# Performance work log

Measured on AMD Instinct MI355X. Metric: run time of the kernel, lower is better.

Reference implementation:

```python
import jax, jax.numpy as jnp
import numpy as np

IN_F = 4096
OUT_F = 11008
RANK = 16
LORA_SCALE = 2.0
VALS_PER_WORD = 16


def pack_int2(T):
    """Pack ternary T in {-1,0,+1} [out, in] into int32 [out, in//16] (code = T+1)."""
    out_f, in_f = T.shape
    codes = (T + 1).astype(jnp.int32).reshape(out_f, in_f // VALS_PER_WORD, VALS_PER_WORD)
    shifts = (jnp.arange(VALS_PER_WORD, dtype=jnp.int32) * 2)
    # disjoint bit fields -> sum == bitwise OR
    return jnp.sum(codes << shifts, axis=-1).astype(jnp.int32)


def unpack_int2(packed, in_features, dtype):
    """Unpack int32 [out, nblk] -> ternary [out, in_features] in given dtype."""
    shifts = (jnp.arange(VALS_PER_WORD, dtype=jnp.int32) * 2)
    codes = (packed[:, :, None] >> shifts) & 3  # [out, nblk, 16]
    T = codes.reshape(packed.shape[0], -1)[:, :in_features]
    return T.astype(dtype) - jnp.asarray(1, dtype)


def setup_inputs() -> dict:
    key = jax.random.key(0)
    k_x, k_t, k_a, k_m, k_b, k_la, k_lb = jax.random.split(key, 7)
    x = jax.random.normal(k_x, (256, IN_F), dtype=jnp.float32)
    # random ternary weights, packed faithfully (code = T + 1)
    T = jax.random.randint(k_t, (OUT_F, IN_F), -1, 2, dtype=jnp.int32)
    int2_packed = pack_int2(T)
    alpha = jax.random.uniform(k_a, (OUT_F,), dtype=jnp.float32, minval=0.01, maxval=0.05)
    mu = jax.random.normal(k_m, (OUT_F,), dtype=jnp.float32) * 0.001
    bias = jax.random.normal(k_b, (OUT_F,), dtype=jnp.float32) * 0.02
    lora_A = jax.random.normal(k_la, (RANK, IN_F), dtype=jnp.float32) * (1.0 / np.sqrt(IN_F))
    lora_B = jax.random.normal(k_lb, (OUT_F, RANK), dtype=jnp.float32) * 0.01
    return {"x": x, "int2_packed": int2_packed, "alpha": alpha, "mu": mu,
            "bias": bias, "lora_A": lora_A, "lora_B": lora_B}


def reference(x, int2_packed, alpha, mu, bias, lora_A, lora_B):
    # unpack INT2 -> ternary weight matrix in activation dtype
    T = unpack_int2(int2_packed, IN_F, x.dtype)          # [out, in]
    ternary_out = jnp.einsum('mi,oi->mo', x, T)          # F.linear(x, T)
    ternary_out = ternary_out * alpha                    # per-row scale
    # asymmetric shift: mu_o * sum_i x_i
    ternary_out = ternary_out + mu * jnp.sum(x, axis=-1, keepdims=True)
    # LoRA correction: scale * (x A^T) B^T
    lora_out = jnp.einsum('mr,or->mo', jnp.einsum('mi,ri->mr', x, lora_A), lora_B)
    ternary_out = ternary_out + LORA_SCALE * lora_out
    return ternary_out + bias
```

## Files before the change

### kernel.cpp

```cpp
#include <hip/hip_runtime.h>
#include <stdint.h>

#define IN_F 4096
#define OUT_F 11008
#define M_ROWS 256
#define RANK 16
#define NWORDS 256

#define BM 128
#define BN 64
#define BK 64
#define KSPLIT 2
#define K_PER 2048
#define NIT 32

typedef unsigned short u16;
typedef __attribute__((ext_vector_type(8))) short short8;
typedef __attribute__((ext_vector_type(4))) float floatx4;

__device__ __forceinline__ u16 f32_to_bf16_rne(float f) {
    uint32_t u = __builtin_bit_cast(uint32_t, f);
    uint32_t r = (u + 0x7FFFu + ((u >> 16) & 1u)) >> 16;
    return (u16)r;
}

__global__ __launch_bounds__(256) void prep_kernel(
    const float* __restrict__ x, const float* __restrict__ lora_A,
    u16* __restrict__ xb, float* __restrict__ srow, float* __restrict__ lxa)
{
    const int m = blockIdx.x;
    const int tid = threadIdx.x;
    const float4* xrow4 = (const float4*)(x + (size_t)m * IN_F);
    const float4* la4 = (const float4*)lora_A;
    float ssum = 0.f;
    float acc[RANK];
#pragma unroll
    for (int r = 0; r < RANK; ++r) acc[r] = 0.f;
#pragma unroll
    for (int t = 0; t < IN_F / (256 * 4); ++t) {
        int i4 = t * 256 + tid;
        float4 v = xrow4[i4];
        ssum += v.x + v.y + v.z + v.w;
        union { u16 h[4]; uint2 u2; } pk;
        pk.h[0] = f32_to_bf16_rne(v.x);
        pk.h[1] = f32_to_bf16_rne(v.y);
        pk.h[2] = f32_to_bf16_rne(v.z);
        pk.h[3] = f32_to_bf16_rne(v.w);
        *(uint2*)&xb[(size_t)m * IN_F + i4 * 4] = pk.u2;
#pragma unroll
        for (int r = 0; r < RANK; ++r) {
            float4 a = la4[r * (IN_F / 4) + i4];
            acc[r] = fmaf(v.x, a.x, fmaf(v.y, a.y, fmaf(v.z, a.z, fmaf(v.w, a.w, acc[r]))));
        }
    }
#pragma unroll
    for (int off = 32; off > 0; off >>= 1) {
        ssum += __shfl_down(ssum, off, 64);
#pragma unroll
        for (int r = 0; r < RANK; ++r) acc[r] += __shfl_down(acc[r], off, 64);
    }
    __shared__ float red[4][RANK + 1];
    int wv = tid >> 6, ln = tid & 63;
    if (ln == 0) {
        red[wv][0] = ssum;
#pragma unroll
        for (int r = 0; r < RANK; ++r) red[wv][1 + r] = acc[r];
    }
    __syncthreads();
    if (tid == 0) srow[m] = red[0][0] + red[1][0] + red[2][0] + red[3][0];
    if (tid < RANK)
        lxa[m * RANK + tid] = red[0][1 + tid] + red[1][1 + tid] + red[2][1 + tid] + red[3][1 + tid];
}

__global__ __launch_bounds__(256) void init_kernel(
    const float* __restrict__ mu,
    const float* __restrict__ bias, const float* __restrict__ lora_B,
    const float* __restrict__ srow, const float* __restrict__ lxa,
    float* __restrict__ out)
{
    const int tid = threadIdx.x;
    const int o = blockIdx.x * 256 + tid;
    const int m0 = blockIdx.y * 32;
    float bi = bias[o];
    float muv = mu[o];
    float Br[RANK];
    const float4* b4 = (const float4*)(lora_B + (size_t)o * RANK);
#pragma unroll
    for (int r4 = 0; r4 < RANK / 4; ++r4) {
        float4 v = b4[r4];
        Br[r4 * 4 + 0] = v.x; Br[r4 * 4 + 1] = v.y;
        Br[r4 * 4 + 2] = v.z; Br[r4 * 4 + 3] = v.w;
    }
    __shared__ float ss[32];
    __shared__ float slx[32][RANK];
    if (tid < 32) ss[tid] = srow[m0 + tid];
    for (int t = tid; t < 32 * RANK; t += 256)
        slx[t >> 4][t & 15] = lxa[(m0 + (t >> 4)) * RANK + (t & 15)];
    __syncthreads();
#pragma unroll 4
    for (int mm = 0; mm < 32; ++mm) {
        float dot = 0.f;
#pragma unroll
        for (int r = 0; r < RANK; ++r) dot = fmaf(slx[mm][r], Br[r], dot);
        out[(size_t)(m0 + mm) * OUT_F + o] = bi + muv * ss[mm] + 2.0f * dot;
    }
}

__device__ __forceinline__ short8 decode8(uint32_t h)
{
    uint32_t selA = (h & 0xFu) | ((h & 0xF0u) << 12);
    selA = (selA | (selA << 6)) & 0x03030303u;
    uint32_t h2 = h >> 8;
    uint32_t selB = (h2 & 0xFu) | ((h2 & 0xF0u) << 12);
    selB = (selB | (selB << 6)) & 0x03030303u;
    uint32_t hiA = __builtin_amdgcn_perm(0u, 0x003F00BFu, selA);
    uint32_t loA = __builtin_amdgcn_perm(0u, 0x00800080u, selA);
    uint32_t hiB = __builtin_amdgcn_perm(0u, 0x003F00BFu, selB);
    uint32_t loB = __builtin_amdgcn_perm(0u, 0x00800080u, selB);
    union { uint32_t u[4]; short8 s; } cvt;
    cvt.u[0] = __builtin_amdgcn_perm(hiA, loA, 0x05010400u);
    cvt.u[1] = __builtin_amdgcn_perm(hiA, loA, 0x07030602u);
    cvt.u[2] = __builtin_amdgcn_perm(hiB, loB, 0x05010400u);
    cvt.u[3] = __builtin_amdgcn_perm(hiB, loB, 0x07030602u);
    return cvt.s;
}

#define WAITV5 asm volatile("s_waitcnt vmcnt(5)" ::: "memory")
#define WAITV0 asm volatile("s_waitcnt vmcnt(0)" ::: "memory")
#define BAR    __builtin_amdgcn_s_barrier()
#define SCHED0 __builtin_amdgcn_sched_barrier(0)

struct Frags {
    short8 af[4][2];
    uint32_t bwd[2][2];
};

__global__ __launch_bounds__(256, 3) void gemm_kernel(
    const u16* __restrict__ xb, const uint32_t* __restrict__ Tp,
    const float* __restrict__ alpha, float* __restrict__ out)
{
    __shared__ __align__(16) u16 ldsA[3][BM * BK];
    __shared__ __align__(16) uint32_t ldsB[3][BN * 4];

    const int tid = threadIdx.x;
    const int lane = tid & 63;
    const int wave = tid >> 6;
    const int wm = wave >> 1, wn = wave & 1;
    const int mb = blockIdx.y * BM;
    const int nb = blockIdx.x * BN;
    const int z = blockIdx.z;

    const int bshift = ((lane >> 4) & 1) * 16;

    const u16* asrc[4];
    int adst[4];
#pragma unroll
    for (int i = 0; i < 4; ++i) {
        int q = i * 256 + tid;
        int row = q >> 3;
        int scc = (q & 7) ^ (row & 7);
        asrc[i] = xb + (size_t)(mb + row) * IN_F + z * K_PER + scc * 8;
        adst[i] = q * 8;
    }
    const uint32_t* bsrc = Tp + (size_t)(nb + lane) * NWORDS + z * (K_PER / 16);
    const int bdst = lane * 4;

    int aoff[4][2], boff[2][2];
#pragma unroll
    for (int mt = 0; mt < 4; ++mt)
#pragma unroll
        for (int kk = 0; kk < 2; ++kk) {
            int r = wm * 64 + mt * 16 + (lane & 15);
            int sc = kk * 4 + (lane >> 4);
            aoff[mt][kk] = (r * 8 + (sc ^ (r & 7))) * 8;
        }
#pragma unroll
    for (int nt = 0; nt < 2; ++nt)
#pragma unroll
        for (int kk = 0; kk < 2; ++kk) {
            int row = wn * 32 + nt * 16 + (lane & 15);
            boff[nt][kk] = row * 4 + kk * 2 + (lane >> 5);
        }

    floatx4 acc[4][2] = {};

    auto stage = [&](int buf, int jt) {
#pragma unroll
        for (int i = 0; i < 4; ++i) {
            __builtin_amdgcn_global_load_lds(
                (const __attribute__((address_space(1))) void*)(asrc[i] + jt * BK),
                (__attribute__((address_space(3))) void*)(&ldsA[buf][adst[i]]),
                16, 0, 0);
        }
        __builtin_amdgcn_global_load_lds(
            (const __attribute__((address_space(1))) void*)(bsrc + jt * 4),
            (__attribute__((address_space(3))) void*)(&ldsB[buf][bdst]),
            16, 0, 0);
    };

    auto rdfrags = [&](int buf, Frags& F) {
#pragma unroll
        for (int mt = 0; mt < 4; ++mt)
#pragma unroll
            for (int kk = 0; kk < 2; ++kk)
                F.af[mt][kk] = *(const short8*)&ldsA[buf][aoff[mt][kk]];
#pragma unroll
        for (int nt = 0; nt < 2; ++nt)
#pragma unroll
            for (int kk = 0; kk < 2; ++kk)
                F.bwd[nt][kk] = ldsB[buf][boff[nt][kk]];
    };

    auto compute = [&](Frags& F) {
        __builtin_amdgcn_s_setprio(1);
#pragma unroll
        for (int kk = 0; kk < 2; ++kk) {
#pragma unroll
            for (int nt = 0; nt < 2; ++nt) {
                short8 bf = decode8((F.bwd[nt][kk] >> bshift) & 0xFFFFu);
#pragma unroll
                for (int mt = 0; mt < 4; ++mt)
                    acc[mt][nt] = __builtin_amdgcn_mfma_f32_16x16x32_bf16(
                        F.af[mt][kk], bf, acc[mt][nt], 0, 0, 0);
            }
        }
        __builtin_amdgcn_s_setprio(0);
    };

    Frags fA, fB;

    stage(0, 0);
    stage(1, 1);
    WAITV5; BAR;
    rdfrags(0, fA); SCHED0;

#pragma unroll 1
    for (int u = 0; u < 5; ++u) {
        const int j = u * 6;
        stage(2, j + 2); SCHED0; compute(fA); WAITV5; BAR; rdfrags(1, fB); SCHED0;
        stage(0, j + 3); SCHED0; compute(fB); WAITV5; BAR; rdfrags(2, fA); SCHED0;
        stage(1, j + 4); SCHED0; compute(fA); WAITV5; BAR; rdfrags(0, fB); SCHED0;
        stage(2, j + 5); SCHED0; compute(fB); WAITV5; BAR; rdfrags(1, fA); SCHED0;
        stage(0, j + 6); SCHED0; compute(fA); WAITV5; BAR; rdfrags(2, fB); SCHED0;
        stage(1, j + 7); SCHED0; compute(fB); WAITV5; BAR; rdfrags(0, fA); SCHED0;
    }
    WAITV0; compute(fA); BAR; rdfrags(1, fB); SCHED0;
    compute(fB);

    const int o0 = nb + wn * 32 + (lane & 15);
    const int m0 = mb + wm * 64 + ((lane >> 4) * 4);
    float al[2] = { alpha[o0], alpha[o0 + 16] };
#pragma unroll
    for (int mt = 0; mt < 4; ++mt) {
#pragma unroll
        for (int rg = 0; rg < 4; ++rg) {
            int m = m0 + mt * 16 + rg;
#pragma unroll
            for (int nt = 0; nt < 2; ++nt)
                atomicAdd(&out[(size_t)m * OUT_F + o0 + nt * 16],
                          al[nt] * acc[mt][nt][rg]);
        }
    }
}

extern "C" void kernel_launch(void* const* d_in, const int* in_sizes, int n_in,
                              void* d_out, int out_size, void* d_ws, size_t ws_size,
                              hipStream_t stream)
{
    const float* x = (const float*)d_in[0];
    const uint32_t* Tp = (const uint32_t*)d_in[1];
    const float* alpha = (const float*)d_in[2];
    const float* mu = (const float*)d_in[3];
    const float* bias = (const float*)d_in[4];
    const float* lora_A = (const float*)d_in[5];
    const float* lora_B = (const float*)d_in[6];
    float* out = (float*)d_out;

    u16* xb = (u16*)d_ws;
    float* srow = (float*)((char*)d_ws + (size_t)M_ROWS * IN_F * 2);
    float* lxa = (float*)((char*)d_ws + (size_t)M_ROWS * IN_F * 2 + 4096);

    prep_kernel<<<dim3(M_ROWS), dim3(256), 0, stream>>>(x, lora_A, xb, srow, lxa);
    init_kernel<<<dim3(OUT_F / 256, M_ROWS / 32), dim3(256), 0, stream>>>(
        mu, bias, lora_B, srow, lxa, out);
    gemm_kernel<<<dim3(OUT_F / BN, M_ROWS / BM, KSPLIT), dim3(256), 0, stream>>>(
        xb, Tp, alpha, out);
}
```

Baseline: 66.04 us.

## Transpose packed weights into coalesced layout, load B to registers, fuse epilogue

A new pack kernel runs on every call and re-lays the packed ternary weights so that consecutive output columns are contiguous per k-word pair. The GEMM can then read B fragments straight from global memory into registers instead of staging them through LDS. The separate init kernel is replaced by a memset plus a fused epilogue in the z==0 split, which adds mu*rowsum, the LoRA term and the bias before its atomic add. This drops the full-output init write pass and the LDS traffic for B, but adds a transpose kernel and a memset each call and lengthens the epilogue of half the blocks.

```diff
diff --git a/kernel.cpp b/kernel.cpp
--- a/kernel.cpp
+++ b/kernel.cpp
@@ -72,37 +72,27 @@
         lxa[m * RANK + tid] = red[0][1 + tid] + red[1][1 + tid] + red[2][1 + tid] + red[3][1 + tid];
 }
 
-__global__ __launch_bounds__(256) void init_kernel(
-    const float* __restrict__ mu,
-    const float* __restrict__ bias, const float* __restrict__ lora_B,
-    const float* __restrict__ srow, const float* __restrict__ lxa,
-    float* __restrict__ out)
-{
+__global__ __launch_bounds__(256) void pack_kernel(
+    const uint32_t* __restrict__ Tp, uint2* __restrict__ Tw2)
+{
+    __shared__ uint32_t s[64][NWORDS + 1];
     const int tid = threadIdx.x;
-    const int o = blockIdx.x * 256 + tid;
-    const int m0 = blockIdx.y * 32;
-    float bi = bias[o];
-    float muv = mu[o];
-    float Br[RANK];
-    const float4* b4 = (const float4*)(lora_B + (size_t)o * RANK);
-#pragma unroll
-    for (int r4 = 0; r4 < RANK / 4; ++r4) {
-        float4 v = b4[r4];
-        Br[r4 * 4 + 0] = v.x; Br[r4 * 4 + 1] = v.y;
-        Br[r4 * 4 + 2] = v.z; Br[r4 * 4 + 3] = v.w;
-    }
-    __shared__ float ss[32];
-    __shared__ float slx[32][RANK];
-    if (tid < 32) ss[tid] = srow[m0 + tid];
-    for (int t = tid; t < 32 * RANK; t += 256)
-        slx[t >> 4][t & 15] = lxa[(m0 + (t >> 4)) * RANK + (t & 15)];
+    const int col0 = blockIdx.x * 64;
+#pragma unroll 8
+    for (int i = 0; i < 64; ++i) {
+        int idx = i * 256 + tid;
+        s[idx >> 8][idx & 255] = Tp[(size_t)(col0 + (idx >> 8)) * NWORDS + (idx & 255)];
+    }
     __syncthreads();
-#pragma unroll 4
-    for (int mm = 0; mm < 32; ++mm) {
-        float dot = 0.f;
-#pragma unroll
-        for (int r = 0; r < RANK; ++r) dot = fmaf(slx[mm][r], Br[r], dot);
-        out[(size_t)(m0 + mm) * OUT_F + o] = bi + muv * ss[mm] + 2.0f * dot;
+    const int c = tid & 63;
+#pragma unroll 8
+    for (int q = 0; q < 32; ++q) {
+        int wq = q * 4 + (tid >> 6);
+        int t = wq >> 1, p = wq & 1;
+        uint2 v;
+        v.x = s[c][4 * t + p];
+        v.y = s[c][4 * t + 2 + p];
+        Tw2[(size_t)wq * OUT_F + col0 + c] = v;
     }
 }
 
@@ -125,22 +115,22 @@
     return cvt.s;
 }
 
-#define WAITV5 asm volatile("s_waitcnt vmcnt(5)" ::: "memory")
+#define WAITV6 asm volatile("s_waitcnt vmcnt(6)" ::: "memory")
 #define WAITV0 asm volatile("s_waitcnt vmcnt(0)" ::: "memory")
 #define BAR    __builtin_amdgcn_s_barrier()
 #define SCHED0 __builtin_amdgcn_sched_barrier(0)
 
-struct Frags {
-    short8 af[4][2];
-    uint32_t bwd[2][2];
-};
+struct Frags { short8 af[4][2]; };
+struct BW    { uint2 w[2]; };
 
 __global__ __launch_bounds__(256, 3) void gemm_kernel(
-    const u16* __restrict__ xb, const uint32_t* __restrict__ Tp,
-    const float* __restrict__ alpha, float* __restrict__ out)
+    const u16* __restrict__ xb, const uint2* __restrict__ Tw2,
+    const float* __restrict__ alpha, const float* __restrict__ mu,
+    const float* __restrict__ bias, const float* __restrict__ lora_B,
+    const float* __restrict__ srow, const float* __restrict__ lxa,
+    float* __restrict__ out)
 {
     __shared__ __align__(16) u16 ldsA[3][BM * BK];
-    __shared__ __align__(16) uint32_t ldsB[3][BN * 4];
 
     const int tid = threadIdx.x;
     const int lane = tid & 63;
@@ -162,10 +152,13 @@
         asrc[i] = xb + (size_t)(mb + row) * IN_F + z * K_PER + scc * 8;
         adst[i] = q * 8;
     }
-    const uint32_t* bsrc = Tp + (size_t)(nb + lane) * NWORDS + z * (K_PER / 16);
-    const int bdst = lane * 4;
-
-    int aoff[4][2], boff[2][2];
+    const uint2* bptr[2];
+#pragma unroll
+    for (int nt = 0; nt < 2; ++nt)
+        bptr[nt] = Tw2 + (size_t)(z * 64 + (lane >> 5)) * OUT_F
+                       + nb + wn * 32 + nt * 16 + (lane & 15);
+
+    int aoff[4][2];
 #pragma unroll
     for (int mt = 0; mt < 4; ++mt)
 #pragma unroll
@@ -173,13 +166,6 @@
             int r = wm * 64 + mt * 16 + (lane & 15);
             int sc = kk * 4 + (lane >> 4);
             aoff[mt][kk] = (r * 8 + (sc ^ (r & 7))) * 8;
-        }
-#pragma unroll
-    for (int nt = 0; nt < 2; ++nt)
-#pragma unroll
-        for (int kk = 0; kk < 2; ++kk) {
-            int row = wn * 32 + nt * 16 + (lane & 15);
-            boff[nt][kk] = row * 4 + kk * 2 + (lane >> 5);
         }
 
     floatx4 acc[4][2] = {};
@@ -192,32 +178,27 @@
                 (__attribute__((address_space(3))) void*)(&ldsA[buf][adst[i]]),
                 16, 0, 0);
         }
-        __builtin_amdgcn_global_load_lds(
-            (const __attribute__((address_space(1))) void*)(bsrc + jt * 4),
-            (__attribute__((address_space(3))) void*)(&ldsB[buf][bdst]),
-            16, 0, 0);
     };
-
+    auto loadB = [&](BW& b, int jt) {
+#pragma unroll
+        for (int nt = 0; nt < 2; ++nt)
+            b.w[nt] = bptr[nt][(size_t)(2 * jt) * OUT_F];
+    };
     auto rdfrags = [&](int buf, Frags& F) {
 #pragma unroll
         for (int mt = 0; mt < 4; ++mt)
 #pragma unroll
             for (int kk = 0; kk < 2; ++kk)
                 F.af[mt][kk] = *(const short8*)&ldsA[buf][aoff[mt][kk]];
-#pragma unroll
-        for (int nt = 0; nt < 2; ++nt)
-#pragma unroll
-            for (int kk = 0; kk < 2; ++kk)
-                F.bwd[nt][kk] = ldsB[buf][boff[nt][kk]];
     };
-
-    auto compute = [&](Frags& F) {
+    auto compute = [&](Frags& F, BW& b) {
         __builtin_amdgcn_s_setprio(1);
 #pragma unroll
         for (int kk = 0; kk < 2; ++kk) {
 #pragma unroll
             for (int nt = 0; nt < 2; ++nt) {
-                short8 bf = decode8((F.bwd[nt][kk] >> bshift) & 0xFFFFu);
+                uint32_t w = kk ? b.w[nt].y : b.w[nt].x;
+                short8 bf = decode8((w >> bshift) & 0xFFFFu);
 #pragma unroll
                 for (int mt = 0; mt < 4; ++mt)
                     acc[mt][nt] = __builtin_amdgcn_mfma_f32_16x16x32_bf16(
@@ -228,37 +209,79 @@
     };
 
     Frags fA, fB;
-
-    stage(0, 0);
-    stage(1, 1);
-    WAITV5; BAR;
+    BW bw0, bw1, bw2;
+
+    stage(0, 0); loadB(bw0, 0);
+    WAITV0; BAR;
     rdfrags(0, fA); SCHED0;
+    loadB(bw1, 1); stage(1, 1);
 
 #pragma unroll 1
     for (int u = 0; u < 5; ++u) {
         const int j = u * 6;
-        stage(2, j + 2); SCHED0; compute(fA); WAITV5; BAR; rdfrags(1, fB); SCHED0;
-        stage(0, j + 3); SCHED0; compute(fB); WAITV5; BAR; rdfrags(2, fA); SCHED0;
-        stage(1, j + 4); SCHED0; compute(fA); WAITV5; BAR; rdfrags(0, fB); SCHED0;
-        stage(2, j + 5); SCHED0; compute(fB); WAITV5; BAR; rdfrags(1, fA); SCHED0;
-        stage(0, j + 6); SCHED0; compute(fA); WAITV5; BAR; rdfrags(2, fB); SCHED0;
-        stage(1, j + 7); SCHED0; compute(fB); WAITV5; BAR; rdfrags(0, fA); SCHED0;
-    }
-    WAITV0; compute(fA); BAR; rdfrags(1, fB); SCHED0;
-    compute(fB);
+        loadB(bw2, j + 2); stage(2, j + 2); SCHED0; compute(fA, bw0); WAITV6; BAR; rdfrags(1, fB); SCHED0;
+        loadB(bw0, j + 3); stage(0, j + 3); SCHED0; compute(fB, bw1); WAITV6; BAR; rdfrags(2, fA); SCHED0;
+        loadB(bw1, j + 4); stage(1, j + 4); SCHED0; compute(fA, bw2); WAITV6; BAR; rdfrags(0, fB); SCHED0;
+        loadB(bw2, j + 5); stage(2, j + 5); SCHED0; compute(fB, bw0); WAITV6; BAR; rdfrags(1, fA); SCHED0;
+        loadB(bw0, j + 6); stage(0, j + 6); SCHED0; compute(fA, bw1); WAITV6; BAR; rdfrags(2, fB); SCHED0;
+        loadB(bw1, j + 7); stage(1, j + 7); SCHED0; compute(fB, bw2); WAITV6; BAR; rdfrags(0, fA); SCHED0;
+    }
+    compute(fA, bw0); WAITV0; BAR; rdfrags(1, fB); SCHED0;
+    compute(fB, bw1);
 
     const int o0 = nb + wn * 32 + (lane & 15);
     const int m0 = mb + wm * 64 + ((lane >> 4) * 4);
     float al[2] = { alpha[o0], alpha[o0 + 16] };
-#pragma unroll
-    for (int mt = 0; mt < 4; ++mt) {
-#pragma unroll
-        for (int rg = 0; rg < 4; ++rg) {
-            int m = m0 + mt * 16 + rg;
-#pragma unroll
-            for (int nt = 0; nt < 2; ++nt)
-                atomicAdd(&out[(size_t)m * OUT_F + o0 + nt * 16],
-                          al[nt] * acc[mt][nt][rg]);
+
+    if (z == 0) {
+        float muv[2] = { mu[o0], mu[o0 + 16] };
+        float bi[2]  = { bias[o0], bias[o0 + 16] };
+        float Brow[2][RANK];
+#pragma unroll
+        for (int nt = 0; nt < 2; ++nt) {
+            const float4* b4 = (const float4*)(lora_B + (size_t)(o0 + nt * 16) * RANK);
+#pragma unroll
+            for (int r4 = 0; r4 < RANK / 4; ++r4) {
+                float4 v = b4[r4];
+                Brow[nt][r4 * 4 + 0] = v.x; Brow[nt][r4 * 4 + 1] = v.y;
+                Brow[nt][r4 * 4 + 2] = v.z; Brow[nt][r4 * 4 + 3] = v.w;
+            }
+        }
+#pragma unroll
+        for (int mt = 0; mt < 4; ++mt) {
+#pragma unroll
+            for (int rg = 0; rg < 4; ++rg) {
+                int m = m0 + mt * 16 + rg;
+                float sm = srow[m];
+                float lx[RANK];
+                const float4* l4 = (const float4*)(lxa + (size_t)m * RANK);
+#pragma unroll
+                for (int r4 = 0; r4 < RANK / 4; ++r4) {
+                    float4 v = l4[r4];
+                    lx[r4 * 4 + 0] = v.x; lx[r4 * 4 + 1] = v.y;
+                    lx[r4 * 4 + 2] = v.z; lx[r4 * 4 + 3] = v.w;
+                }
+#pragma unroll
+                for (int nt = 0; nt < 2; ++nt) {
+                    float lora = 0.f;
+#pragma unroll
+                    for (int r = 0; r < RANK; ++r) lora = fmaf(lx[r], Brow[nt][r], lora);
+                    atomicAdd(&out[(size_t)m * OUT_F + o0 + nt * 16],
+                              al[nt] * acc[mt][nt][rg] + muv[nt] * sm + 2.0f * lora + bi[nt]);
+                }
+            }
+        }
+    } else {
+#pragma unroll
+        for (int mt = 0; mt < 4; ++mt) {
+#pragma unroll
+            for (int rg = 0; rg < 4; ++rg) {
+                int m = m0 + mt * 16 + rg;
+#pragma unroll
+                for (int nt = 0; nt < 2; ++nt)
+                    atomicAdd(&out[(size_t)m * OUT_F + o0 + nt * 16],
+                              al[nt] * acc[mt][nt][rg]);
+            }
         }
     }
 }
@@ -279,10 +302,11 @@
     u16* xb = (u16*)d_ws;
     float* srow = (float*)((char*)d_ws + (size_t)M_ROWS * IN_F * 2);
     float* lxa = (float*)((char*)d_ws + (size_t)M_ROWS * IN_F * 2 + 4096);
-
+    uint2* Tw2 = (uint2*)((char*)d_ws + (4u << 20));
+
+    hipMemsetAsync(out, 0, (size_t)out_size * sizeof(float), stream);
     prep_kernel<<<dim3(M_ROWS), dim3(256), 0, stream>>>(x, lora_A, xb, srow, lxa);
-    init_kernel<<<dim3(OUT_F / 256, M_ROWS / 32), dim3(256), 0, stream>>>(
-        mu, bias, lora_B, srow, lxa, out);
+    pack_kernel<<<dim3(OUT_F / 64), dim3(256), 0, stream>>>(Tp, Tw2);
     gemm_kernel<<<dim3(OUT_F / BN, M_ROWS / BM, KSPLIT), dim3(256), 0, stream>>>(
-        xb, Tp, alpha, out);
-}
+        xb, Tw2, alpha, mu, bias, lora_B, srow, lxa, out);
+}
```

After: 73.54 us. +11.4%, slower.

## Repack ternary weights for direct register loads and widen GEMM tiles

Applied to the files above, without the earlier changes.

Adds a pack kernel that transposes the packed INT2 weights into a column-interleaved uint2 layout, so GEMM waves can load B words straight from global into registers instead of staging them through LDS. The GEMM tile widens to BN=128, split-K rises to 4 with a 4-deep A ring buffer, and occupancy drops to 2 blocks per SM. The repack runs on every call, which adds a kernel launch and extra weight traffic, and split-K 4 doubles the atomic output traffic.

```diff
diff --git a/kernel.cpp b/kernel.cpp
--- a/kernel.cpp
+++ b/kernel.cpp
@@ -8,11 +8,11 @@
 #define NWORDS 256
 
 #define BM 128
-#define BN 64
+#define BN 128
 #define BK 64
-#define KSPLIT 2
-#define K_PER 2048
-#define NIT 32
+#define KSPLIT 4
+#define K_PER 1024
+#define NIT 16
 
 typedef unsigned short u16;
 typedef __attribute__((ext_vector_type(8))) short short8;
@@ -70,6 +70,30 @@
     if (tid == 0) srow[m] = red[0][0] + red[1][0] + red[2][0] + red[3][0];
     if (tid < RANK)
         lxa[m * RANK + tid] = red[0][1 + tid] + red[1][1 + tid] + red[2][1 + tid] + red[3][1 + tid];
+}
+
+__global__ __launch_bounds__(256) void pack_kernel(
+    const uint32_t* __restrict__ Tp, uint2* __restrict__ Tw2)
+{
+    __shared__ uint32_t s[64][NWORDS + 1];
+    const int tid = threadIdx.x;
+    const int col0 = blockIdx.x * 64;
+#pragma unroll 8
+    for (int i = 0; i < 64; ++i) {
+        int idx = i * 256 + tid;
+        s[idx >> 8][idx & 255] = Tp[(size_t)(col0 + (idx >> 8)) * NWORDS + (idx & 255)];
+    }
+    __syncthreads();
+    const int c = tid & 63;
+#pragma unroll 8
+    for (int q = 0; q < 32; ++q) {
+        int wq = q * 4 + (tid >> 6);
+        int t = wq >> 1, p = wq & 1;
+        uint2 v;
+        v.x = s[c][4 * t + p];
+        v.y = s[c][4 * t + 2 + p];
+        Tw2[(size_t)wq * OUT_F + col0 + c] = v;
+    }
 }
 
 __global__ __launch_bounds__(256) void init_kernel(
@@ -125,22 +149,18 @@
     return cvt.s;
 }
 
-#define WAITV5 asm volatile("s_waitcnt vmcnt(5)" ::: "memory")
-#define WAITV0 asm volatile("s_waitcnt vmcnt(0)" ::: "memory")
+#define WAITV(N) asm volatile("s_waitcnt vmcnt(" #N ")" ::: "memory")
 #define BAR    __builtin_amdgcn_s_barrier()
 #define SCHED0 __builtin_amdgcn_sched_barrier(0)
 
-struct Frags {
-    short8 af[4][2];
-    uint32_t bwd[2][2];
-};
-
-__global__ __launch_bounds__(256, 3) void gemm_kernel(
-    const u16* __restrict__ xb, const uint32_t* __restrict__ Tp,
+struct Frags { short8 af[4][2]; };
+struct BW    { uint2 w[4]; };
+
+__global__ __launch_bounds__(256, 2) void gemm_kernel(
+    const u16* __restrict__ xb, const uint2* __restrict__ Tw2,
     const float* __restrict__ alpha, float* __restrict__ out)
 {
-    __shared__ __align__(16) u16 ldsA[3][BM * BK];
-    __shared__ __align__(16) uint32_t ldsB[3][BN * 4];
+    __shared__ __align__(16) u16 ldsA[4][BM * BK];
 
     const int tid = threadIdx.x;
     const int lane = tid & 63;
@@ -162,10 +182,13 @@
         asrc[i] = xb + (size_t)(mb + row) * IN_F + z * K_PER + scc * 8;
         adst[i] = q * 8;
     }
-    const uint32_t* bsrc = Tp + (size_t)(nb + lane) * NWORDS + z * (K_PER / 16);
-    const int bdst = lane * 4;
-
-    int aoff[4][2], boff[2][2];
+    const uint2* bptr[4];
+#pragma unroll
+    for (int nt = 0; nt < 4; ++nt)
+        bptr[nt] = Tw2 + (size_t)(z * 32 + (lane >> 5)) * OUT_F
+                       + nb + wn * 64 + nt * 16 + (lane & 15);
+
+    int aoff[4][2];
 #pragma unroll
     for (int mt = 0; mt < 4; ++mt)
 #pragma unroll
@@ -174,15 +197,8 @@
             int sc = kk * 4 + (lane >> 4);
             aoff[mt][kk] = (r * 8 + (sc ^ (r & 7))) * 8;
         }
-#pragma unroll
-    for (int nt = 0; nt < 2; ++nt)
-#pragma unroll
-        for (int kk = 0; kk < 2; ++kk) {
-            int row = wn * 32 + nt * 16 + (lane & 15);
-            boff[nt][kk] = row * 4 + kk * 2 + (lane >> 5);
-        }
-
-    floatx4 acc[4][2] = {};
+
+    floatx4 acc[4][4] = {};
 
     auto stage = [&](int buf, int jt) {
 #pragma unroll
@@ -192,32 +208,27 @@
                 (__attribute__((address_space(3))) void*)(&ldsA[buf][adst[i]]),
                 16, 0, 0);
         }
-        __builtin_amdgcn_global_load_lds(
-            (const __attribute__((address_space(1))) void*)(bsrc + jt * 4),
-            (__attribute__((address_space(3))) void*)(&ldsB[buf][bdst]),
-            16, 0, 0);
     };
-
+    auto loadB = [&](BW& b, int jt) {
+#pragma unroll
+        for (int nt = 0; nt < 4; ++nt)
+            b.w[nt] = bptr[nt][(size_t)(2 * jt) * OUT_F];
+    };
     auto rdfrags = [&](int buf, Frags& F) {
 #pragma unroll
         for (int mt = 0; mt < 4; ++mt)
 #pragma unroll
             for (int kk = 0; kk < 2; ++kk)
                 F.af[mt][kk] = *(const short8*)&ldsA[buf][aoff[mt][kk]];
-#pragma unroll
-        for (int nt = 0; nt < 2; ++nt)
-#pragma unroll
-            for (int kk = 0; kk < 2; ++kk)
-                F.bwd[nt][kk] = ldsB[buf][boff[nt][kk]];
     };
-
-    auto compute = [&](Frags& F) {
+    auto compute = [&](Frags& F, BW& b) {
         __builtin_amdgcn_s_setprio(1);
 #pragma unroll
         for (int kk = 0; kk < 2; ++kk) {
 #pragma unroll
-            for (int nt = 0; nt < 2; ++nt) {
-                short8 bf = decode8((F.bwd[nt][kk] >> bshift) & 0xFFFFu);
+            for (int nt = 0; nt < 4; ++nt) {
+                uint32_t w = kk ? b.w[nt].y : b.w[nt].x;
+                short8 bf = decode8((w >> bshift) & 0xFFFFu);
 #pragma unroll
                 for (int mt = 0; mt < 4; ++mt)
                     acc[mt][nt] = __builtin_amdgcn_mfma_f32_16x16x32_bf16(
@@ -227,36 +238,41 @@
         __builtin_amdgcn_s_setprio(0);
     };
 
-    Frags fA, fB;
-
-    stage(0, 0);
-    stage(1, 1);
-    WAITV5; BAR;
-    rdfrags(0, fA); SCHED0;
-
-#pragma unroll 1
-    for (int u = 0; u < 5; ++u) {
-        const int j = u * 6;
-        stage(2, j + 2); SCHED0; compute(fA); WAITV5; BAR; rdfrags(1, fB); SCHED0;
-        stage(0, j + 3); SCHED0; compute(fB); WAITV5; BAR; rdfrags(2, fA); SCHED0;
-        stage(1, j + 4); SCHED0; compute(fA); WAITV5; BAR; rdfrags(0, fB); SCHED0;
-        stage(2, j + 5); SCHED0; compute(fB); WAITV5; BAR; rdfrags(1, fA); SCHED0;
-        stage(0, j + 6); SCHED0; compute(fA); WAITV5; BAR; rdfrags(2, fB); SCHED0;
-        stage(1, j + 7); SCHED0; compute(fB); WAITV5; BAR; rdfrags(0, fA); SCHED0;
-    }
-    WAITV0; compute(fA); BAR; rdfrags(1, fB); SCHED0;
-    compute(fB);
-
-    const int o0 = nb + wn * 32 + (lane & 15);
+    Frags f0, f1;
+    BW bw[3];
+
+    stage(0, 0); stage(1, 1); stage(2, 2);
+    loadB(bw[0], 0); loadB(bw[1], 1);
+    WAITV(16); BAR;
+    rdfrags(0, f0); SCHED0;
+
+#pragma unroll
+    for (int j = 0; j <= 12; ++j) {
+        loadB(bw[(j + 2) % 3], j + 2);
+        stage((j + 3) & 3, j + 3); SCHED0;
+        WAITV(12);
+        if ((j & 1) == 0) { compute(f0, bw[j % 3]); } else { compute(f1, bw[j % 3]); }
+        BAR;
+        if ((j & 1) == 0) { rdfrags((j + 1) & 3, f1); } else { rdfrags((j + 1) & 3, f0); }
+        SCHED0;
+    }
+    loadB(bw[0], 15); SCHED0;
+    WAITV(12); compute(f1, bw[1]); BAR; rdfrags(2, f0); SCHED0;
+    WAITV(4); compute(f0, bw[2]); BAR; rdfrags(3, f1); SCHED0;
+    WAITV(0); compute(f1, bw[0]);
+
+    const int o0 = nb + wn * 64 + (lane & 15);
     const int m0 = mb + wm * 64 + ((lane >> 4) * 4);
-    float al[2] = { alpha[o0], alpha[o0 + 16] };
+    float al[4];
+#pragma unroll
+    for (int nt = 0; nt < 4; ++nt) al[nt] = alpha[o0 + nt * 16];
 #pragma unroll
     for (int mt = 0; mt < 4; ++mt) {
 #pragma unroll
         for (int rg = 0; rg < 4; ++rg) {
             int m = m0 + mt * 16 + rg;
 #pragma unroll
-            for (int nt = 0; nt < 2; ++nt)
+            for (int nt = 0; nt < 4; ++nt)
                 atomicAdd(&out[(size_t)m * OUT_F + o0 + nt * 16],
                           al[nt] * acc[mt][nt][rg]);
         }
@@ -279,10 +295,12 @@
     u16* xb = (u16*)d_ws;
     float* srow = (float*)((char*)d_ws + (size_t)M_ROWS * IN_F * 2);
     float* lxa = (float*)((char*)d_ws + (size_t)M_ROWS * IN_F * 2 + 4096);
+    uint2* Tw2 = (uint2*)((char*)d_ws + (4u << 20));
 
     prep_kernel<<<dim3(M_ROWS), dim3(256), 0, stream>>>(x, lora_A, xb, srow, lxa);
+    pack_kernel<<<dim3(OUT_F / 64), dim3(256), 0, stream>>>(Tp, Tw2);
     init_kernel<<<dim3(OUT_F / 256, M_ROWS / 32), dim3(256), 0, stream>>>(
         mu, bias, lora_B, srow, lxa, out);
     gemm_kernel<<<dim3(OUT_F / BN, M_ROWS / BM, KSPLIT), dim3(256), 0, stream>>>(
-        xb, Tp, alpha, out);
-}
+        xb, Tw2, alpha, out);
+}
```

New measurement: 95.05 us. +43.9%, slower.
